# Optimization experiments

Measured on AMD Instinct MI355X. Metric: run time of the kernel, lower is better.

Reference implementation:

```python
import jax, jax.numpy as jnp
import numpy as np

EPS = 1e-5
NHEAD = 8
TOP_K = 2


def _layernorm(x, g, b):
    m = jnp.mean(x, axis=-1, keepdims=True)
    v = jnp.mean((x - m) ** 2, axis=-1, keepdims=True)
    return (x - m) * jax.lax.rsqrt(v + EPS) * g + b


def setup_inputs() -> dict:
    S, D, F, E = 4096, 512, 2048, 8
    key = jax.random.key(0)
    ks = jax.random.split(key, 18)
    std = 0.02
    return {
        "src": jax.random.normal(ks[0], (S, D), jnp.float32),
        "in_proj_w": std * jax.random.normal(ks[1], (3 * D, D), jnp.float32),
        "in_proj_b": jnp.zeros((3 * D,), jnp.float32),
        "out_proj_w": std * jax.random.normal(ks[2], (D, D), jnp.float32),
        "out_proj_b": jnp.zeros((D,), jnp.float32),
        "ln1_g": jnp.ones((D,), jnp.float32),
        "ln1_b": jnp.zeros((D,), jnp.float32),
        "ln2_g": jnp.ones((D,), jnp.float32),
        "ln2_b": jnp.zeros((D,), jnp.float32),
        "gate_w": std * jax.random.normal(ks[3], (E, D), jnp.float32),
        "gate_b": jnp.zeros((E,), jnp.float32),
        "w1": std * jax.random.normal(ks[4], (E, F, D), jnp.float32),
        "b1": jnp.zeros((E, F), jnp.float32),
        "w2": std * jax.random.normal(ks[5], (E, F, D), jnp.float32),
        "b2": jnp.zeros((E, F), jnp.float32),
        "wo": std * jax.random.normal(ks[6], (E, D, F), jnp.float32),
        "bo": jnp.zeros((E, D), jnp.float32),
    }


def _sa_block(x, in_proj_w, in_proj_b, out_proj_w, out_proj_b):
    # x: [S, D] unbatched sequence (torch MultiheadAttention unbatched path)
    S, D = x.shape
    hd = D // NHEAD
    qkv = x @ in_proj_w.T + in_proj_b              # [S, 3D]
    q, k, v = jnp.split(qkv, 3, axis=-1)
    q = q.reshape(S, NHEAD, hd)
    k = k.reshape(S, NHEAD, hd)
    v = v.reshape(S, NHEAD, hd)
    scores = jnp.einsum("shd,thd->hst", q, k) / jnp.sqrt(jnp.float32(hd))
    attn = jax.nn.softmax(scores, axis=-1)         # [H, S, S]
    out = jnp.einsum("hst,thd->shd", attn, v).reshape(S, D)
    return out @ out_proj_w.T + out_proj_b


def _ff_block(x, gate_w, gate_b, w1, b1, w2, b2, wo, bo):
    # top-k gated SwiGLU MoE; gate probs are softmax, NOT renormalized after topk
    T = x.shape[0]
    E = w1.shape[0]
    gates = jax.nn.softmax(x @ gate_w.T + gate_b, axis=-1)      # [T, E]
    top_scores, top_idx = jax.lax.top_k(gates, TOP_K)            # [T, k]
    combine = jnp.zeros((T, E), x.dtype).at[
        jnp.arange(T)[:, None], top_idx].add(top_scores)         # [T, E]
    out = jnp.zeros_like(x)
    for e in range(E):  # small fixed expert count
        h = jax.nn.silu(x @ w1[e].T + b1[e]) * (x @ w2[e].T + b2[e])
        out = out + combine[:, e:e + 1] * (h @ wo[e].T + bo[e])
    return out


def reference(src, in_proj_w, in_proj_b, out_proj_w, out_proj_b,
              ln1_g, ln1_b, ln2_g, ln2_b,
              gate_w, gate_b, w1, b1, w2, b2, wo, bo):
    # norm_first pre-norm residual layer, dropout=0 (eval)
    x = src
    x = x + _sa_block(_layernorm(x, ln1_g, ln1_b),
                      in_proj_w, in_proj_b, out_proj_w, out_proj_b)
    x = x + _ff_block(_layernorm(x, ln2_g, ln2_b),
                      gate_w, gate_b, w1, b1, w2, b2, wo, bo)
    return x
```

## Files before the change

kernel.cpp:

```cpp
#include <hip/hip_runtime.h>
#include <hip/hip_bf16.h>
#include <math.h>

#define SQ   4096
#define DM   512
#define NH   8
#define HDIM 64
#define FF   2048
#define NE   8

typedef unsigned short u16;
typedef unsigned int   u32;
typedef __attribute__((ext_vector_type(8))) __bf16 bf16x8;
typedef __attribute__((ext_vector_type(4))) float  f32x4;

__device__ __forceinline__ float bf2f(u16 v) {
    union { u32 i; float f; } c; c.i = ((u32)v) << 16; return c.f;
}
__device__ __forceinline__ u16 f2bf(float f) {
    union { __bf16 h; u16 u; } c; c.h = (__bf16)f; return c.u;
}

#define BM 128
#define BN 128
#define BK 32
#define BKP 40

__global__ __launch_bounds__(256) void gemm_split(
    const u16* __restrict__ Ahi, const u16* __restrict__ Alo, int lda,
    const u16* __restrict__ Bhi, const u16* __restrict__ Blo, int ldb,
    int M, int N, int K,
    const float* __restrict__ bias,
    const float* __restrict__ resid, int ldres,
    u16* __restrict__ Chi, u16* __restrict__ Clo,
    float* __restrict__ Cf, int ldc, int mode)
{
    __shared__ __align__(16) u16 Ash[BM * BKP], Asl[BM * BKP];
    __shared__ __align__(16) u16 Bsh[BN * BKP], Bsl[BN * BKP];
    const int tid  = threadIdx.x;
    const int wave = tid >> 6;
    const int lane = tid & 63;
    const int quad = lane >> 4;
    const int l16  = lane & 15;
    const int bm = blockIdx.x * BM;
    const int bn = blockIdx.y * BN;
    const int wm = (wave & 1) * 64;
    const int wn = (wave >> 1) * 64;

    f32x4 acc[4][4];
#pragma unroll
    for (int i = 0; i < 4; i++)
#pragma unroll
        for (int j = 0; j < 4; j++)
#pragma unroll
            for (int r = 0; r < 4; r++) acc[i][j][r] = 0.0f;

    for (int k0 = 0; k0 < K; k0 += BK) {
#pragma unroll
        for (int i = 0; i < 2; i++) {
            int c = tid + i * 256;
            int row = c >> 2;
            int col = (c & 3) << 3;
            int ga = bm + row, gb2 = bn + row;
            uint4 vah = make_uint4(0u,0u,0u,0u), val = vah, vbh = vah, vbl = vah;
            if (ga < M) {
                vah = *(const uint4*)(Ahi + (size_t)ga * lda + k0 + col);
                val = *(const uint4*)(Alo + (size_t)ga * lda + k0 + col);
            }
            if (gb2 < N) {
                vbh = *(const uint4*)(Bhi + (size_t)gb2 * ldb + k0 + col);
                vbl = *(const uint4*)(Blo + (size_t)gb2 * ldb + k0 + col);
            }
            *(uint4*)(Ash + row * BKP + col) = vah;
            *(uint4*)(Asl + row * BKP + col) = val;
            *(uint4*)(Bsh + row * BKP + col) = vbh;
            *(uint4*)(Bsl + row * BKP + col) = vbl;
        }
        __syncthreads();
        bf16x8 ah[4], al[4], bh[4], bl[4];
#pragma unroll
        for (int i = 0; i < 4; i++) {
            ah[i] = *(const bf16x8*)(Ash + (wm + i * 16 + l16) * BKP + quad * 8);
            al[i] = *(const bf16x8*)(Asl + (wm + i * 16 + l16) * BKP + quad * 8);
        }
#pragma unroll
        for (int j = 0; j < 4; j++) {
            bh[j] = *(const bf16x8*)(Bsh + (wn + j * 16 + l16) * BKP + quad * 8);
            bl[j] = *(const bf16x8*)(Bsl + (wn + j * 16 + l16) * BKP + quad * 8);
        }
#pragma unroll
        for (int i = 0; i < 4; i++)
#pragma unroll
            for (int j = 0; j < 4; j++) {
                acc[i][j] = __builtin_amdgcn_mfma_f32_16x16x32_bf16(ah[i], bh[j], acc[i][j], 0,0,0);
                acc[i][j] = __builtin_amdgcn_mfma_f32_16x16x32_bf16(ah[i], bl[j], acc[i][j], 0,0,0);
                acc[i][j] = __builtin_amdgcn_mfma_f32_16x16x32_bf16(al[i], bh[j], acc[i][j], 0,0,0);
            }
        __syncthreads();
    }

#pragma unroll
    for (int i = 0; i < 4; i++)
#pragma unroll
        for (int j = 0; j < 4; j++)
#pragma unroll
            for (int r = 0; r < 4; r++) {
                int row = bm + wm + i * 16 + quad * 4 + r;
                int col = bn + wn + j * 16 + l16;
                if (row >= M || col >= N) continue;
                float v = acc[i][j][r] + (bias ? bias[col] : 0.0f);
                size_t idx = (size_t)row * ldc + col;
                if (mode == 0) {
                    u16 hb = f2bf(v);
                    Chi[idx] = hb;
                    Clo[idx] = f2bf(v - bf2f(hb));
                } else {
                    if (resid) v += resid[(size_t)row * ldres + col];
                    Cf[idx] = v;
                }
            }
}

__global__ __launch_bounds__(256) void moe12_all(
    const u16* __restrict__ A, int lda,
    const int* __restrict__ idxl, const int* __restrict__ cnt,
    const int* __restrict__ off,
    const float* __restrict__ w1, const float* __restrict__ b1,
    const float* __restrict__ w2, const float* __restrict__ b2,
    u16* __restrict__ H)
{
    const int bmg = blockIdx.x * BM;
    if (bmg >= off[NE]) return;
    int e = 0;
    while (e < NE - 1 && bmg >= off[e + 1]) e++;
    const int M   = cnt[e];
    const int bml = bmg - off[e];
    if (bml >= M) return;
    const float* B1 = w1 + (size_t)e * FF * DM;
    const float* B2 = w2 + (size_t)e * FF * DM;
    const int*   rl = idxl + e * SQ;

    __shared__ __align__(16) u16 As[BM * BKP], Bs1[BN * BKP], Bs2[BN * BKP];
    const int tid  = threadIdx.x;
    const int wave = tid >> 6;
    const int lane = tid & 63;
    const int quad = lane >> 4;
    const int l16  = lane & 15;
    const int bn = blockIdx.y * BN;
    const int wm = (wave & 1) * 64;
    const int wn = (wave >> 1) * 64;

    f32x4 acc1[4][4], acc2[4][4];
#pragma unroll
    for (int i = 0; i < 4; i++)
#pragma unroll
        for (int j = 0; j < 4; j++)
#pragma unroll
            for (int r = 0; r < 4; r++) { acc1[i][j][r] = 0.0f; acc2[i][j][r] = 0.0f; }

    for (int k0 = 0; k0 < DM; k0 += BK) {
#pragma unroll
        for (int i = 0; i < 2; i++) {
            int c = tid + i * 256;
            int row = c >> 2;
            int col = (c & 3) << 3;
            uint4 va = make_uint4(0u,0u,0u,0u);
            int lr = bml + row;
            if (lr < M) {
                int ar = rl[lr];
                va = *(const uint4*)(A + (size_t)ar * lda + k0 + col);
            }
            *(uint4*)(As + row * BKP + col) = va;
        }
#pragma unroll
        for (int i = 0; i < 4; i++) {
            int c = tid + i * 256;
            int row = c >> 3;
            int col = (c & 7) << 2;
            float4 v1 = *(const float4*)(B1 + (size_t)(bn + row) * DM + k0 + col);
            float4 v2 = *(const float4*)(B2 + (size_t)(bn + row) * DM + k0 + col);
            ushort4 h1, h2;
            h1.x = f2bf(v1.x); h1.y = f2bf(v1.y); h1.z = f2bf(v1.z); h1.w = f2bf(v1.w);
            h2.x = f2bf(v2.x); h2.y = f2bf(v2.y); h2.z = f2bf(v2.z); h2.w = f2bf(v2.w);
            *(ushort4*)(Bs1 + row * BKP + col) = h1;
            *(ushort4*)(Bs2 + row * BKP + col) = h2;
        }
        __syncthreads();
        bf16x8 af[4], b1f[4], b2f[4];
#pragma unroll
        for (int i = 0; i < 4; i++)
            af[i] = *(const bf16x8*)(As + (wm + i * 16 + l16) * BKP + quad * 8);
#pragma unroll
        for (int j = 0; j < 4; j++) {
            b1f[j] = *(const bf16x8*)(Bs1 + (wn + j * 16 + l16) * BKP + quad * 8);
            b2f[j] = *(const bf16x8*)(Bs2 + (wn + j * 16 + l16) * BKP + quad * 8);
        }
#pragma unroll
        for (int i = 0; i < 4; i++)
#pragma unroll
            for (int j = 0; j < 4; j++) {
                acc1[i][j] = __builtin_amdgcn_mfma_f32_16x16x32_bf16(af[i], b1f[j], acc1[i][j], 0,0,0);
                acc2[i][j] = __builtin_amdgcn_mfma_f32_16x16x32_bf16(af[i], b2f[j], acc2[i][j], 0,0,0);
            }
        __syncthreads();
    }

#pragma unroll
    for (int i = 0; i < 4; i++)
#pragma unroll
        for (int j = 0; j < 4; j++)
#pragma unroll
            for (int r = 0; r < 4; r++) {
                int rowl = bml + wm + i * 16 + quad * 4 + r;
                if (rowl >= M) continue;
                int col = bn + wn + j * 16 + l16;
                float g1 = acc1[i][j][r] + b1[e * FF + col];
                float g2 = acc2[i][j][r] + b2[e * FF + col];
                float s  = g1 / (1.0f + __expf(-g1));
                H[(size_t)(off[e] + rowl) * FF + col] = f2bf(s * g2);
            }
}

__global__ __launch_bounds__(256) void moe_y_all(
    const u16* __restrict__ H,
    const float* __restrict__ wo, const float* __restrict__ bo,
    const int* __restrict__ idxl, const float* __restrict__ cw,
    const int* __restrict__ cnt, const int* __restrict__ off,
    float* __restrict__ out)
{
    const int bmg = blockIdx.x * BM;
    if (bmg >= off[NE]) return;
    int e = 0;
    while (e < NE - 1 && bmg >= off[e + 1]) e++;
    const int M   = cnt[e];
    const int bml = bmg - off[e];
    if (bml >= M) return;
    const float* B = wo + (size_t)e * DM * FF;

    __shared__ __align__(16) u16 As[BM * BKP], Bs[BN * BKP];
    const int tid  = threadIdx.x;
    const int wave = tid >> 6;
    const int lane = tid & 63;
    const int quad = lane >> 4;
    const int l16  = lane & 15;
    const int bn = blockIdx.y * BN;
    const int wm = (wave & 1) * 64;
    const int wn = (wave >> 1) * 64;

    f32x4 acc[4][4];
#pragma unroll
    for (int i = 0; i < 4; i++)
#pragma unroll
        for (int j = 0; j < 4; j++)
#pragma unroll
            for (int r = 0; r < 4; r++) acc[i][j][r] = 0.0f;

    for (int k0 = 0; k0 < FF; k0 += BK) {
#pragma unroll
        for (int i = 0; i < 2; i++) {
            int c = tid + i * 256;
            int row = c >> 2;
            int col = (c & 3) << 3;
            uint4 va = *(const uint4*)(H + (size_t)(bmg + row) * FF + k0 + col);
            *(uint4*)(As + row * BKP + col) = va;
        }
#pragma unroll
        for (int i = 0; i < 4; i++) {
            int c = tid + i * 256;
            int row = c >> 3;
            int col = (c & 7) << 2;
            float4 v = *(const float4*)(B + (size_t)(bn + row) * FF + k0 + col);
            ushort4 h;
            h.x = f2bf(v.x); h.y = f2bf(v.y); h.z = f2bf(v.z); h.w = f2bf(v.w);
            *(ushort4*)(Bs + row * BKP + col) = h;
        }
        __syncthreads();
        bf16x8 af[4], bf[4];
#pragma unroll
        for (int i = 0; i < 4; i++)
            af[i] = *(const bf16x8*)(As + (wm + i * 16 + l16) * BKP + quad * 8);
#pragma unroll
        for (int j = 0; j < 4; j++)
            bf[j] = *(const bf16x8*)(Bs + (wn + j * 16 + l16) * BKP + quad * 8);
#pragma unroll
        for (int i = 0; i < 4; i++)
#pragma unroll
            for (int j = 0; j < 4; j++)
                acc[i][j] = __builtin_amdgcn_mfma_f32_16x16x32_bf16(af[i], bf[j], acc[i][j], 0,0,0);
        __syncthreads();
    }

#pragma unroll
    for (int i = 0; i < 4; i++)
#pragma unroll
        for (int j = 0; j < 4; j++)
#pragma unroll
            for (int r = 0; r < 4; r++) {
                int rowl = bml + wm + i * 16 + quad * 4 + r;
                if (rowl >= M) continue;
                int col = bn + wn + j * 16 + l16;
                int tok = idxl[e * SQ + rowl];
                float wgt = cw[e * SQ + rowl];
                atomicAdd(out + (size_t)tok * DM + col,
                          wgt * (acc[i][j][r] + bo[e * DM + col]));
            }
}

#define KP 64
#define SWZ(row, col) ((col) ^ (((row) & 7) << 3))
#define SCL 0.18033688011112042f

template <int SPLIT>
__device__ __forceinline__ void flash_body(
    const u16* __restrict__ qh, const u16* __restrict__ ql,
    const u16* __restrict__ vth, const u16* __restrict__ vtl,
    u16* __restrict__ oh, u16* __restrict__ ol,
    float* __restrict__ Opart, float* __restrict__ mpart,
    float* __restrict__ lpart)
{
    __shared__ __align__(16) u16 Ksh[64*KP], Ksl[64*KP], Vsh[64*KP], Vsl[64*KP];
    const int tid  = threadIdx.x;
    const int wave = tid >> 6;
    const int lane = tid & 63;
    const int quad = lane >> 4;
    const int l16  = lane & 15;
    const int h    = blockIdx.y;
    const int z    = (SPLIT > 1) ? blockIdx.z : 0;
    const int qbase = blockIdx.x * 64 + wave * 16;

    u16* const Pwh = Ksh + wave * (16 * KP);
    u16* const Pwl = Ksl + wave * (16 * KP);

    const int r_st  = tid >> 3;
    const int co_g  = (tid & 7) << 3;
    const int co_sw = SWZ(r_st, co_g);

    bf16x8 aqh[2], aql[2];
#pragma unroll
    for (int kk = 0; kk < 2; kk++) {
        size_t off = (size_t)(qbase + l16) * (3*DM) + h*HDIM + kk*32 + quad*8;
        aqh[kk] = *(const bf16x8*)(qh + off);
        aql[kk] = *(const bf16x8*)(ql + off);
    }

    float m_[4], l_[4];
    f32x4 o_[4];
#pragma unroll
    for (int r = 0; r < 4; r++) { m_[r] = -1e30f; l_[r] = 0.0f; }
#pragma unroll
    for (int nd = 0; nd < 4; nd++)
#pragma unroll
        for (int r = 0; r < 4; r++) o_[nd][r] = 0.0f;

    const int NT    = SQ / 64 / SPLIT;
    const int jtBeg = z * NT, jtEnd = (z + 1) * NT;

    for (int jt = jtBeg; jt < jtEnd; jt++) {
        {
            size_t koff0 = (size_t)(jt*64 + r_st) * (3*DM) + DM + h*HDIM + co_g;
            size_t voff0 = (size_t)(h*HDIM + r_st) * SQ + jt*64 + co_g;
            size_t koff1 = koff0 + (size_t)32 * (3*DM);
            size_t voff1 = voff0 + (size_t)32 * SQ;
            uint4 a0 = *(const uint4*)(qh  + koff0);
            uint4 a1 = *(const uint4*)(ql  + koff0);
            uint4 a2 = *(const uint4*)(vth + voff0);
            uint4 a3 = *(const uint4*)(vtl + voff0);
            uint4 b0 = *(const uint4*)(qh  + koff1);
            uint4 b1 = *(const uint4*)(ql  + koff1);
            uint4 b2 = *(const uint4*)(vth + voff1);
            uint4 b3 = *(const uint4*)(vtl + voff1);
            *(uint4*)(Ksh + r_st*KP + co_sw)      = a0;
            *(uint4*)(Ksl + r_st*KP + co_sw)      = a1;
            *(uint4*)(Vsh + r_st*KP + co_sw)      = a2;
            *(uint4*)(Vsl + r_st*KP + co_sw)      = a3;
            *(uint4*)(Ksh + (r_st+32)*KP + co_sw) = b0;
            *(uint4*)(Ksl + (r_st+32)*KP + co_sw) = b1;
            *(uint4*)(Vsh + (r_st+32)*KP + co_sw) = b2;
            *(uint4*)(Vsl + (r_st+32)*KP + co_sw) = b3;
        }
        __syncthreads();

        f32x4 s[4];
        __builtin_amdgcn_s_setprio(1);
#pragma unroll
        for (int jn = 0; jn < 4; jn++) {
            f32x4 zz;
#pragma unroll
            for (int r = 0; r < 4; r++) zz[r] = 0.0f;
#pragma unroll
            for (int kk = 0; kk < 2; kk++) {
                int krow = jn*16 + l16;
                int kcol = SWZ(krow, kk*32 + quad*8);
                bf16x8 kh = *(const bf16x8*)(Ksh + krow*KP + kcol);
                bf16x8 kl = *(const bf16x8*)(Ksl + krow*KP + kcol);
                zz = __builtin_amdgcn_mfma_f32_16x16x32_bf16(aqh[kk], kh, zz, 0,0,0);
                zz = __builtin_amdgcn_mfma_f32_16x16x32_bf16(aqh[kk], kl, zz, 0,0,0);
                zz = __builtin_amdgcn_mfma_f32_16x16x32_bf16(aql[kk], kh, zz, 0,0,0);
            }
#pragma unroll
            for (int r = 0; r < 4; r++) zz[r] *= SCL;
            s[jn] = zz;
        }
        __builtin_amdgcn_s_setprio(0);
        __syncthreads();

        float mx[4];
#pragma unroll
        for (int r = 0; r < 4; r++) {
            mx[r] = fmaxf(fmaxf(s[0][r], s[1][r]), fmaxf(s[2][r], s[3][r]));
#pragma unroll
            for (int o2 = 1; o2 < 16; o2 <<= 1)
                mx[r] = fmaxf(mx[r], __shfl_xor(mx[r], o2));
        }
        int grew = (mx[0] > m_[0] + 8.0f) | (mx[1] > m_[1] + 8.0f) |
                   (mx[2] > m_[2] + 8.0f) | (mx[3] > m_[3] + 8.0f);
        if (__any(grew)) {
#pragma unroll
            for (int r = 0; r < 4; r++) {
                float nm  = fmaxf(m_[r], mx[r]);
                float al2 = exp2f(m_[r] - nm);
                m_[r] = nm;
                l_[r] *= al2;
#pragma unroll
                for (int nd = 0; nd < 4; nd++) o_[nd][r] *= al2;
            }
        }
        float rs[4];
#pragma unroll
        for (int r = 0; r < 4; r++) rs[r] = 0.0f;
#pragma unroll
        for (int jn = 0; jn < 4; jn++)
#pragma unroll
            for (int r = 0; r < 4; r++) {
                float p = exp2f(s[jn][r] - m_[r]);
                s[jn][r] = p;
                rs[r] += p;
            }
#pragma unroll
        for (int r = 0; r < 4; r++) {
#pragma unroll
            for (int o2 = 1; o2 < 16; o2 <<= 1)
                rs[r] += __shfl_xor(rs[r], o2);
            l_[r] += rs[r];
        }
#pragma unroll
        for (int jn = 0; jn < 4; jn++)
#pragma unroll
            for (int r = 0; r < 4; r++) {
                float p = s[jn][r];
                u16 ph = f2bf(p);
                int rr   = quad*4 + r;
                int pidx = rr*KP + SWZ(rr, jn*16 + l16);
                Pwh[pidx] = ph;
                Pwl[pidx] = f2bf(p - bf2f(ph));
            }

        bf16x8 ph[2], pl[2];
#pragma unroll
        for (int kk = 0; kk < 2; kk++) {
            int pcol = SWZ(l16, kk*32 + quad*8);
            ph[kk] = *(const bf16x8*)(Pwh + l16*KP + pcol);
            pl[kk] = *(const bf16x8*)(Pwl + l16*KP + pcol);
        }
        __builtin_amdgcn_s_setprio(1);
#pragma unroll
        for (int nd = 0; nd < 4; nd++) {
#pragma unroll
            for (int kk = 0; kk < 2; kk++) {
                int vrow = nd*16 + l16;
                int vcol = SWZ(vrow, kk*32 + quad*8);
                bf16x8 vh = *(const bf16x8*)(Vsh + vrow*KP + vcol);
                bf16x8 vl = *(const bf16x8*)(Vsl + vrow*KP + vcol);
                o_[nd] = __builtin_amdgcn_mfma_f32_16x16x32_bf16(ph[kk], vh, o_[nd], 0,0,0);
                o_[nd] = __builtin_amdgcn_mfma_f32_16x16x32_bf16(ph[kk], vl, o_[nd], 0,0,0);
                o_[nd] = __builtin_amdgcn_mfma_f32_16x16x32_bf16(pl[kk], vh, o_[nd], 0,0,0);
            }
        }
        __builtin_amdgcn_s_setprio(0);
        __syncthreads();
    }

    if (SPLIT == 1) {
#pragma unroll
        for (int nd = 0; nd < 4; nd++)
#pragma unroll
            for (int r = 0; r < 4; r++) {
                int row = qbase + quad*4 + r;
                int col = h*HDIM + nd*16 + l16;
                float w = o_[nd][r] / l_[r];
                u16 hb = f2bf(w);
                oh[(size_t)row * DM + col] = hb;
                ol[(size_t)row * DM + col] = f2bf(w - bf2f(hb));
            }
    } else {
#pragma unroll
        for (int nd = 0; nd < 4; nd++)
#pragma unroll
            for (int r = 0; r < 4; r++) {
                int row = qbase + quad*4 + r;
                int col = h*HDIM + nd*16 + l16;
                Opart[((size_t)z * SQ + row) * DM + col] = o_[nd][r];
            }
        if (l16 == 0) {
#pragma unroll
            for (int r = 0; r < 4; r++) {
                int row = qbase + quad*4 + r;
                mpart[(z*NH + h) * SQ + row] = m_[r];
                lpart[(z*NH + h) * SQ + row] = l_[r];
            }
        }
    }
}

__global__ __launch_bounds__(256) void flash_attn(
    const u16* __restrict__ qh, const u16* __restrict__ ql,
    const u16* __restrict__ vth, const u16* __restrict__ vtl,
    u16* __restrict__ oh, u16* __restrict__ ol)
{
    flash_body<1>(qh, ql, vth, vtl, oh, ol, nullptr, nullptr, nullptr);
}

__global__ __launch_bounds__(256) void flash_attn_part2(
    const u16* __restrict__ qh, const u16* __restrict__ ql,
    const u16* __restrict__ vth, const u16* __restrict__ vtl,
    float* __restrict__ Opart, float* __restrict__ mpart,
    float* __restrict__ lpart)
{
    flash_body<2>(qh, ql, vth, vtl, nullptr, nullptr, Opart, mpart, lpart);
}

__global__ __launch_bounds__(256) void flash_attn_part4(
    const u16* __restrict__ qh, const u16* __restrict__ ql,
    const u16* __restrict__ vth, const u16* __restrict__ vtl,
    float* __restrict__ Opart, float* __restrict__ mpart,
    float* __restrict__ lpart)
{
    flash_body<4>(qh, ql, vth, vtl, nullptr, nullptr, Opart, mpart, lpart);
}

__global__ __launch_bounds__(256) void attn_combine(
    const float* __restrict__ Opart, const float* __restrict__ mpart,
    const float* __restrict__ lpart,
    u16* __restrict__ oh, u16* __restrict__ ol, int ns)
{
    const int row = blockIdx.x;
    const int tid = threadIdx.x;
#pragma unroll
    for (int i = 0; i < 2; i++) {
        int col = tid + i * 256;
        int h = col >> 6;
        float m = -1e30f;
        for (int zz = 0; zz < ns; zz++)
            m = fmaxf(m, mpart[(zz*NH + h) * SQ + row]);
        float O = 0.0f, l = 0.0f;
        for (int zz = 0; zz < ns; zz++) {
            float a = exp2f(mpart[(zz*NH + h) * SQ + row] - m);
            O += Opart[((size_t)zz * SQ + row) * DM + col] * a;
            l += lpart[(zz*NH + h) * SQ + row] * a;
        }
        float w = O / l;
        u16 hb = f2bf(w);
        oh[(size_t)row * DM + col] = hb;
        ol[(size_t)row * DM + col] = f2bf(w - bf2f(hb));
    }
}

__global__ __launch_bounds__(256) void ln1_split(
    const float* __restrict__ x, const float* __restrict__ g,
    const float* __restrict__ b, u16* __restrict__ ohi, u16* __restrict__ olo)
{
    const int row = blockIdx.x;
    const int tid = threadIdx.x;
    float v0 = x[(size_t)row * DM + tid];
    float v1 = x[(size_t)row * DM + tid + 256];
    float s = v0 + v1, sq = v0*v0 + v1*v1;
#pragma unroll
    for (int o = 1; o < 64; o <<= 1) { s += __shfl_xor(s, o); sq += __shfl_xor(sq, o); }
    __shared__ float ss[4], ssq[4];
    if ((tid & 63) == 0) { ss[tid>>6] = s; ssq[tid>>6] = sq; }
    __syncthreads();
    s  = ss[0]+ss[1]+ss[2]+ss[3];
    sq = ssq[0]+ssq[1]+ssq[2]+ssq[3];
    float m = s * (1.0f/DM);
    float rstd = rsqrtf(sq*(1.0f/DM) - m*m + 1e-5f);
    float y0 = (v0-m)*rstd*g[tid]     + b[tid];
    float y1 = (v1-m)*rstd*g[tid+256] + b[tid+256];
    u16 h0 = f2bf(y0), h1 = f2bf(y1);
    ohi[(size_t)row*DM + tid]       = h0;  olo[(size_t)row*DM + tid]       = f2bf(y0 - bf2f(h0));
    ohi[(size_t)row*DM + tid + 256] = h1;  olo[(size_t)row*DM + tid + 256] = f2bf(y1 - bf2f(h1));
}

__global__ __launch_bounds__(256) void ln_kernel(
    const float* __restrict__ x, const float* __restrict__ g,
    const float* __restrict__ b, u16* __restrict__ out)
{
    const int row = blockIdx.x;
    const int tid = threadIdx.x;
    float v0 = x[(size_t)row * DM + tid];
    float v1 = x[(size_t)row * DM + tid + 256];
    float s = v0 + v1, sq = v0*v0 + v1*v1;
#pragma unroll
    for (int o = 1; o < 64; o <<= 1) { s += __shfl_xor(s, o); sq += __shfl_xor(sq, o); }
    __shared__ float ss[4], ssq[4];
    if ((tid & 63) == 0) { ss[tid>>6] = s; ssq[tid>>6] = sq; }
    __syncthreads();
    s  = ss[0]+ss[1]+ss[2]+ss[3];
    sq = ssq[0]+ssq[1]+ssq[2]+ssq[3];
    float m = s * (1.0f/DM);
    float rstd = rsqrtf(sq*(1.0f/DM) - m*m + 1e-5f);
    out[(size_t)row*DM + tid]       = f2bf((v0-m)*rstd*g[tid]     + b[tid]);
    out[(size_t)row*DM + tid + 256] = f2bf((v1-m)*rstd*g[tid+256] + b[tid+256]);
}

__global__ __launch_bounds__(256) void transpose_v2(
    const u16* __restrict__ qh, const u16* __restrict__ ql,
    u16* __restrict__ vth, u16* __restrict__ vtl)
{
    __shared__ u16 Th[64 * 66], Tl[64 * 66];
    const int t0  = blockIdx.x * 64;
    const int hd0 = blockIdx.y * 64;
    const int tid = threadIdx.x;
#pragma unroll
    for (int k = 0; k < 16; k++) {
        int idx = tid + k * 256;
        int r = idx >> 6, j = idx & 63;
        size_t src = (size_t)(t0 + r) * (3*DM) + 2*DM + hd0 + j;
        Th[r * 66 + j] = qh[src];
        Tl[r * 66 + j] = ql[src];
    }
    __syncthreads();
#pragma unroll
    for (int k = 0; k < 16; k++) {
        int idx = tid + k * 256;
        int r = idx >> 6, c2 = idx & 63;
        size_t dst = (size_t)(hd0 + r) * SQ + t0 + c2;
        vth[dst] = Th[c2 * 66 + r];
        vtl[dst] = Tl[c2 * 66 + r];
    }
}

__global__ __launch_bounds__(256) void gate_route(
    const float* __restrict__ x1, const float* __restrict__ g,
    const float* __restrict__ b, const float* __restrict__ gw,
    const float* __restrict__ gb,
    int* __restrict__ cnt, int* __restrict__ idxl, float* __restrict__ cw)
{
    const int token = blockIdx.x * 4 + (threadIdx.x >> 6);
    const int lane  = threadIdx.x & 63;
    const float* xr = x1 + (size_t)token * DM;
    float v[8];
#pragma unroll
    for (int i = 0; i < 8; i++) v[i] = xr[lane*8 + i];
    float s = 0.f, sq = 0.f;
#pragma unroll
    for (int i = 0; i < 8; i++) { s += v[i]; sq += v[i]*v[i]; }
#pragma unroll
    for (int o = 1; o < 64; o <<= 1) { s += __shfl_xor(s, o); sq += __shfl_xor(sq, o); }
    float m = s * (1.0f/DM);
    float rstd = rsqrtf(sq*(1.0f/DM) - m*m + 1e-5f);
    float xn[8];
#pragma unroll
    for (int i = 0; i < 8; i++)
        xn[i] = (v[i]-m)*rstd*g[lane*8+i] + b[lane*8+i];
    float logit[8];
#pragma unroll
    for (int e = 0; e < 8; e++) {
        float t = 0.f;
#pragma unroll
        for (int i = 0; i < 8; i++) t += xn[i] * gw[e*DM + lane*8 + i];
#pragma unroll
        for (int o = 1; o < 64; o <<= 1) t += __shfl_xor(t, o);
        logit[e] = t + gb[e];
    }
    if (lane == 0) {
        float mx = -1e30f;
        for (int e = 0; e < 8; e++) mx = fmaxf(mx, logit[e]);
        float den = 0.f, p[8];
        for (int e = 0; e < 8; e++) { p[e] = __expf(logit[e] - mx); den += p[e]; }
        for (int e = 0; e < 8; e++) p[e] /= den;
        int i1 = 0;
        for (int e = 1; e < 8; e++) if (p[e] > p[i1]) i1 = e;
        int i2 = -1;
        for (int e = 0; e < 8; e++) { if (e == i1) continue; if (i2 < 0 || p[e] > p[i2]) i2 = e; }
        int s1 = atomicAdd(&cnt[i1], 1);
        idxl[i1*SQ + s1] = token;  cw[i1*SQ + s1] = p[i1];
        int s2 = atomicAdd(&cnt[i2], 1);
        idxl[i2*SQ + s2] = token;  cw[i2*SQ + s2] = p[i2];
    }
}

__global__ __launch_bounds__(256) void cvt_split_w(
    const float* __restrict__ w, u16* __restrict__ wh, u16* __restrict__ wl, int n)
{
    int i = blockIdx.x * 256 + threadIdx.x;
    if (i < n) {
        float v = w[i];
        u16 h = f2bf(v);
        wh[i] = h;
        wl[i] = f2bf(v - bf2f(h));
    }
}

__global__ __launch_bounds__(64) void zero_cnt(int* cnt)
{
    if (threadIdx.x < NE) cnt[threadIdx.x] = 0;
}

__global__ __launch_bounds__(64) void make_off(const int* __restrict__ cnt,
                                              int* __restrict__ off)
{
    if (threadIdx.x == 0) {
        int a = 0;
        for (int e = 0; e < NE; e++) {
            off[e] = a;
            a += ((cnt[e] + 127) >> 7) << 7;
        }
        off[NE] = a;
    }
}

__global__ __launch_bounds__(256) void init_out(
    const float* __restrict__ x1, float* __restrict__ out)
{
    int i = blockIdx.x * 256 + threadIdx.x;
    ((float4*)out)[i] = ((const float4*)x1)[i];
}

__global__ __launch_bounds__(256) void sentinel_kernel(float* out, float v, int n)
{
    int i = blockIdx.x * 256 + threadIdx.x;
    if (i < n) out[i] = v;
}
__global__ __launch_bounds__(256) void scrub_kernel(float* out, int n)
{
    int i = blockIdx.x * 256 + threadIdx.x;
    if (i < n) { float v = out[i]; if (!isfinite(v)) out[i] = 777.0f; }
}

extern "C" void kernel_launch(void* const* d_in, const int* in_sizes, int n_in,
                              void* d_out, int out_size, void* d_ws, size_t ws_size,
                              hipStream_t stream)
{
    const float* src        = (const float*)d_in[0];
    const float* in_proj_w  = (const float*)d_in[1];
    const float* in_proj_b  = (const float*)d_in[2];
    const float* out_proj_w = (const float*)d_in[3];
    const float* out_proj_b = (const float*)d_in[4];
    const float* ln1_g      = (const float*)d_in[5];
    const float* ln1_b      = (const float*)d_in[6];
    const float* ln2_g      = (const float*)d_in[7];
    const float* ln2_b      = (const float*)d_in[8];
    const float* gate_w     = (const float*)d_in[9];
    const float* gate_b     = (const float*)d_in[10];
    const float* w1         = (const float*)d_in[11];
    const float* b1         = (const float*)d_in[12];
    const float* w2         = (const float*)d_in[13];
    const float* b2         = (const float*)d_in[14];
    const float* wo         = (const float*)d_in[15];
    const float* bo         = (const float*)d_in[16];
    float* out = (float*)d_out;

    const size_t MB = (size_t)1 << 20;
    const size_t ROUTE = 512 * 1024;
    const size_t NEED      = ROUTE + 44 * MB;
    const size_t NEED_BIG2 = ROUTE + 61 * MB;
    const size_t NEED_BIG4 = ROUTE + 78 * MB;
    if (ws_size < NEED) {
        sentinel_kernel<<<(SQ*DM)/256, 256, 0, stream>>>(out, 333.0f, SQ*DM);
        return;
    }
    int ns = 0;
    if (ws_size >= NEED_BIG4)      ns = 4;
    else if (ws_size >= NEED_BIG2) ns = 2;

    char* ws = (char*)d_ws;
    int*   cnt  = (int*)ws;
    int*   offp = (int*)(ws + 64);
    int*   idxl = (int*)(ws + 1024);
    float* cw   = (float*)(ws + 1024 + 128*1024);
    char*  base = ws + ROUTE;
    u16* xln1h = (u16*)(base);
    u16* xln1l = (u16*)(base + 4*MB);
    u16* attnh = (u16*)(base);
    u16* attnl = (u16*)(base + 4*MB);
    u16* qkvh  = (u16*)(base + 8*MB);
    u16* qkvl  = (u16*)(base + 20*MB);
    float* x1  = (float*)(base + 8*MB);
    u16* vth   = (u16*)(base + 32*MB);
    u16* vtl   = (u16*)(base + 36*MB);
    u16* xln2  = (u16*)(base + 36*MB);
    u16* Hbuf  = (u16*)(base);
    u16* wph   = (u16*)(base + 40*MB);
    u16* wpl   = (u16*)(base + 40*MB + 1536*1024);
    u16* woh   = (u16*)(base + 43*MB);
    u16* wol   = (u16*)(base + 43*MB + 512*1024);
    float* Opart = (float*)(base + 44*MB);
    float* mpart;
    float* lpart;
    if (ns == 4) {
        mpart = (float*)(base + 76*MB);
        lpart = (float*)(base + 76*MB + 512*1024);
    } else {
        mpart = (float*)(base + 60*MB);
        lpart = (float*)(base + 60*MB + 256*1024);
    }

    cvt_split_w<<<(3*DM*DM)/256, 256, 0, stream>>>(in_proj_w,  wph, wpl, 3*DM*DM);
    cvt_split_w<<<(DM*DM)/256,   256, 0, stream>>>(out_proj_w, woh, wol, DM*DM);

    ln1_split<<<SQ, 256, 0, stream>>>(src, ln1_g, ln1_b, xln1h, xln1l);
    gemm_split<<<dim3(32, 12), 256, 0, stream>>>(
        xln1h, xln1l, DM, wph, wpl, DM, SQ, 3*DM, DM,
        in_proj_b, nullptr, 0, qkvh, qkvl, nullptr, 3*DM, 0);
    transpose_v2<<<dim3(SQ/64, DM/64), 256, 0, stream>>>(qkvh, qkvl, vth, vtl);
    if (ns == 4) {
        flash_attn_part4<<<dim3(SQ/64, NH, 4), 256, 0, stream>>>(
            qkvh, qkvl, vth, vtl, Opart, mpart, lpart);
        attn_combine<<<SQ, 256, 0, stream>>>(Opart, mpart, lpart, attnh, attnl, 4);
    } else if (ns == 2) {
        flash_attn_part2<<<dim3(SQ/64, NH, 2), 256, 0, stream>>>(
            qkvh, qkvl, vth, vtl, Opart, mpart, lpart);
        attn_combine<<<SQ, 256, 0, stream>>>(Opart, mpart, lpart, attnh, attnl, 2);
    } else {
        flash_attn<<<dim3(SQ/64, NH), 256, 0, stream>>>(
            qkvh, qkvl, vth, vtl, attnh, attnl);
    }
    gemm_split<<<dim3(32, 4), 256, 0, stream>>>(
        attnh, attnl, DM, woh, wol, DM, SQ, DM, DM,
        out_proj_b, src, DM, nullptr, nullptr, x1, DM, 1);

    ln_kernel<<<SQ, 256, 0, stream>>>(x1, ln2_g, ln2_b, xln2);
    zero_cnt<<<1, 64, 0, stream>>>(cnt);
    gate_route<<<SQ/4, 256, 0, stream>>>(x1, ln2_g, ln2_b, gate_w, gate_b,
                                         cnt, idxl, cw);
    make_off<<<1, 64, 0, stream>>>(cnt, offp);
    init_out<<<(SQ*DM/4)/256, 256, 0, stream>>>(x1, out);
    moe12_all<<<dim3(72, 16), 256, 0, stream>>>(
        xln2, DM, idxl, cnt, offp, w1, b1, w2, b2, Hbuf);
    moe_y_all<<<dim3(72, 4), 256, 0, stream>>>(
        Hbuf, wo, bo, idxl, cw, cnt, offp, out);

    scrub_kernel<<<(SQ*DM)/256, 256, 0, stream>>>(out, SQ*DM);
}
```

Before: 794.1 us.

## Pre-convert MoE expert weights to bf16 and split-K the out-projection with atomics

Adds kernels that convert the fp32 expert weights w1, w2 and wo to bf16 once per call, then run bf16-weight variants of the two MoE GEMMs. These replace the older kernels, which read fp32 weights and presumably converted them while loading tiles. The out-projection GEMM is split four ways along K with atomicAdd into x1, which is first initialised with src plus the bias, to raise block count. The trade is extra conversion passes and atomic traffic. The new MoE path runs only when ns==4, and the weight buffers reuse scratch regions that Opart/mpart also use.

```diff
diff --git a/kernel.cpp b/kernel.cpp
--- a/kernel.cpp
+++ b/kernel.cpp
@@ -121,6 +121,96 @@
             }
 }
 
+__global__ __launch_bounds__(256) void gemm_split_ko(
+    const u16* __restrict__ Ahi, const u16* __restrict__ Alo, int lda,
+    const u16* __restrict__ Bhi, const u16* __restrict__ Blo, int ldb,
+    float* __restrict__ Cf, int ldc)
+{
+    __shared__ __align__(16) u16 Ash[BM * BKP], Asl[BM * BKP];
+    __shared__ __align__(16) u16 Bsh[BN * BKP], Bsl[BN * BKP];
+    const int tid  = threadIdx.x;
+    const int wave = tid >> 6;
+    const int lane = tid & 63;
+    const int quad = lane >> 4;
+    const int l16  = lane & 15;
+    const int bm = blockIdx.x * BM;
+    const int bn = blockIdx.y * BN;
+    const int wm = (wave & 1) * 64;
+    const int wn = (wave >> 1) * 64;
+    const int KC    = DM / 4;
+    const int k0beg = blockIdx.z * KC;
+
+    f32x4 acc[4][4];
+#pragma unroll
+    for (int i = 0; i < 4; i++)
+#pragma unroll
+        for (int j = 0; j < 4; j++)
+#pragma unroll
+            for (int r = 0; r < 4; r++) acc[i][j][r] = 0.0f;
+
+    for (int k0 = k0beg; k0 < k0beg + KC; k0 += BK) {
+#pragma unroll
+        for (int i = 0; i < 2; i++) {
+            int c = tid + i * 256;
+            int row = c >> 2;
+            int col = (c & 3) << 3;
+            int ga = bm + row, gb2 = bn + row;
+            uint4 vah = *(const uint4*)(Ahi + (size_t)ga * lda + k0 + col);
+            uint4 val = *(const uint4*)(Alo + (size_t)ga * lda + k0 + col);
+            uint4 vbh = *(const uint4*)(Bhi + (size_t)gb2 * ldb + k0 + col);
+            uint4 vbl = *(const uint4*)(Blo + (size_t)gb2 * ldb + k0 + col);
+            *(uint4*)(Ash + row * BKP + col) = vah;
+            *(uint4*)(Asl + row * BKP + col) = val;
+            *(uint4*)(Bsh + row * BKP + col) = vbh;
+            *(uint4*)(Bsl + row * BKP + col) = vbl;
+        }
+        __syncthreads();
+        bf16x8 ah[4], al[4], bh[4], bl[4];
+#pragma unroll
+        for (int i = 0; i < 4; i++) {
+            ah[i] = *(const bf16x8*)(Ash + (wm + i * 16 + l16) * BKP + quad * 8);
+            al[i] = *(const bf16x8*)(Asl + (wm + i * 16 + l16) * BKP + quad * 8);
+        }
+#pragma unroll
+        for (int j = 0; j < 4; j++) {
+            bh[j] = *(const bf16x8*)(Bsh + (wn + j * 16 + l16) * BKP + quad * 8);
+            bl[j] = *(const bf16x8*)(Bsl + (wn + j * 16 + l16) * BKP + quad * 8);
+        }
+#pragma unroll
+        for (int i = 0; i < 4; i++)
+#pragma unroll
+            for (int j = 0; j < 4; j++) {
+                acc[i][j] = __builtin_amdgcn_mfma_f32_16x16x32_bf16(ah[i], bh[j], acc[i][j], 0,0,0);
+                acc[i][j] = __builtin_amdgcn_mfma_f32_16x16x32_bf16(ah[i], bl[j], acc[i][j], 0,0,0);
+                acc[i][j] = __builtin_amdgcn_mfma_f32_16x16x32_bf16(al[i], bh[j], acc[i][j], 0,0,0);
+            }
+        __syncthreads();
+    }
+
+#pragma unroll
+    for (int i = 0; i < 4; i++)
+#pragma unroll
+        for (int j = 0; j < 4; j++)
+#pragma unroll
+            for (int r = 0; r < 4; r++) {
+                int row = bm + wm + i * 16 + quad * 4 + r;
+                int col = bn + wn + j * 16 + l16;
+                atomicAdd(Cf + (size_t)row * ldc + col, acc[i][j][r]);
+            }
+}
+
+__global__ __launch_bounds__(256) void init_x1(
+    const float* __restrict__ src, const float* __restrict__ bias,
+    float* __restrict__ x1)
+{
+    int i = blockIdx.x * 256 + threadIdx.x;
+    int col4 = i & (DM / 4 - 1);
+    float4 s = ((const float4*)src)[i];
+    float4 b = ((const float4*)bias)[col4];
+    s.x += b.x; s.y += b.y; s.z += b.z; s.w += b.w;
+    ((float4*)x1)[i] = s;
+}
+
 __global__ __launch_bounds__(256) void moe12_all(
     const u16* __restrict__ A, int lda,
     const int* __restrict__ idxl, const int* __restrict__ cnt,
@@ -221,6 +311,97 @@
             }
 }
 
+__global__ __launch_bounds__(256) void moe12_bf16(
+    const u16* __restrict__ A, int lda,
+    const int* __restrict__ idxl, const int* __restrict__ cnt,
+    const int* __restrict__ off,
+    const u16* __restrict__ w1b, const float* __restrict__ b1,
+    const u16* __restrict__ w2b, const float* __restrict__ b2,
+    u16* __restrict__ H)
+{
+    const int bmg = blockIdx.x * BM;
+    if (bmg >= off[NE]) return;
+    int e = 0;
+    while (e < NE - 1 && bmg >= off[e + 1]) e++;
+    const int M   = cnt[e];
+    const int bml = bmg - off[e];
+    if (bml >= M) return;
+    const u16* B1 = w1b + (size_t)e * FF * DM;
+    const u16* B2 = w2b + (size_t)e * FF * DM;
+    const int* rl = idxl + e * SQ;
+
+    __shared__ __align__(16) u16 As[BM * BKP], Bs1[BN * BKP], Bs2[BN * BKP];
+    const int tid  = threadIdx.x;
+    const int wave = tid >> 6;
+    const int lane = tid & 63;
+    const int quad = lane >> 4;
+    const int l16  = lane & 15;
+    const int bn = blockIdx.y * BN;
+    const int wm = (wave & 1) * 64;
+    const int wn = (wave >> 1) * 64;
+
+    f32x4 acc1[4][4], acc2[4][4];
+#pragma unroll
+    for (int i = 0; i < 4; i++)
+#pragma unroll
+        for (int j = 0; j < 4; j++)
+#pragma unroll
+            for (int r = 0; r < 4; r++) { acc1[i][j][r] = 0.0f; acc2[i][j][r] = 0.0f; }
+
+    for (int k0 = 0; k0 < DM; k0 += BK) {
+#pragma unroll
+        for (int i = 0; i < 2; i++) {
+            int c = tid + i * 256;
+            int row = c >> 2;
+            int col = (c & 3) << 3;
+            uint4 va = make_uint4(0u,0u,0u,0u);
+            int lr = bml + row;
+            if (lr < M) {
+                int ar = rl[lr];
+                va = *(const uint4*)(A + (size_t)ar * lda + k0 + col);
+            }
+            *(uint4*)(As + row * BKP + col) = va;
+            uint4 v1 = *(const uint4*)(B1 + (size_t)(bn + row) * DM + k0 + col);
+            uint4 v2 = *(const uint4*)(B2 + (size_t)(bn + row) * DM + k0 + col);
+            *(uint4*)(Bs1 + row * BKP + col) = v1;
+            *(uint4*)(Bs2 + row * BKP + col) = v2;
+        }
+        __syncthreads();
+        bf16x8 af[4], b1f[4], b2f[4];
+#pragma unroll
+        for (int i = 0; i < 4; i++)
+            af[i] = *(const bf16x8*)(As + (wm + i * 16 + l16) * BKP + quad * 8);
+#pragma unroll
+        for (int j = 0; j < 4; j++) {
+            b1f[j] = *(const bf16x8*)(Bs1 + (wn + j * 16 + l16) * BKP + quad * 8);
+            b2f[j] = *(const bf16x8*)(Bs2 + (wn + j * 16 + l16) * BKP + quad * 8);
+        }
+#pragma unroll
+        for (int i = 0; i < 4; i++)
+#pragma unroll
+            for (int j = 0; j < 4; j++) {
+                acc1[i][j] = __builtin_amdgcn_mfma_f32_16x16x32_bf16(af[i], b1f[j], acc1[i][j], 0,0,0);
+                acc2[i][j] = __builtin_amdgcn_mfma_f32_16x16x32_bf16(af[i], b2f[j], acc2[i][j], 0,0,0);
+            }
+        __syncthreads();
+    }
+
+#pragma unroll
+    for (int i = 0; i < 4; i++)
+#pragma unroll
+        for (int j = 0; j < 4; j++)
+#pragma unroll
+            for (int r = 0; r < 4; r++) {
+                int rowl = bml + wm + i * 16 + quad * 4 + r;
+                if (rowl >= M) continue;
+                int col = bn + wn + j * 16 + l16;
+                float g1 = acc1[i][j][r] + b1[e * FF + col];
+                float g2 = acc2[i][j][r] + b2[e * FF + col];
+                float s  = g1 / (1.0f + __expf(-g1));
+                H[(size_t)(off[e] + rowl) * FF + col] = f2bf(s * g2);
+            }
+}
+
 __global__ __launch_bounds__(256) void moe_y_all(
     const u16* __restrict__ H,
     const float* __restrict__ wo, const float* __restrict__ bo,
@@ -304,6 +485,95 @@
                 atomicAdd(out + (size_t)tok * DM + col,
                           wgt * (acc[i][j][r] + bo[e * DM + col]));
             }
+}
+
+__global__ __launch_bounds__(256) void moe_y_bf16(
+    const u16* __restrict__ H,
+    const u16* __restrict__ wob, const float* __restrict__ bo,
+    const int* __restrict__ idxl, const float* __restrict__ cw,
+    const int* __restrict__ cnt, const int* __restrict__ off,
+    float* __restrict__ out)
+{
+    const int bmg = blockIdx.x * BM;
+    if (bmg >= off[NE]) return;
+    int e = 0;
+    while (e < NE - 1 && bmg >= off[e + 1]) e++;
+    const int M   = cnt[e];
+    const int bml = bmg - off[e];
+    if (bml >= M) return;
+    const u16* B = wob + (size_t)e * DM * FF;
+
+    __shared__ __align__(16) u16 As[BM * BKP], Bs[BN * BKP];
+    const int tid  = threadIdx.x;
+    const int wave = tid >> 6;
+    const int lane = tid & 63;
+    const int quad = lane >> 4;
+    const int l16  = lane & 15;
+    const int bn = blockIdx.y * BN;
+    const int wm = (wave & 1) * 64;
+    const int wn = (wave >> 1) * 64;
+
+    f32x4 acc[4][4];
+#pragma unroll
+    for (int i = 0; i < 4; i++)
+#pragma unroll
+        for (int j = 0; j < 4; j++)
+#pragma unroll
+            for (int r = 0; r < 4; r++) acc[i][j][r] = 0.0f;
+
+    for (int k0 = 0; k0 < FF; k0 += BK) {
+#pragma unroll
+        for (int i = 0; i < 2; i++) {
+            int c = tid + i * 256;
+            int row = c >> 2;
+            int col = (c & 3) << 3;
+            uint4 va = *(const uint4*)(H + (size_t)(bmg + row) * FF + k0 + col);
+            *(uint4*)(As + row * BKP + col) = va;
+            uint4 vb = *(const uint4*)(B + (size_t)(bn + row) * FF + k0 + col);
+            *(uint4*)(Bs + row * BKP + col) = vb;
+        }
+        __syncthreads();
+        bf16x8 af[4], bf[4];
+#pragma unroll
+        for (int i = 0; i < 4; i++)
+            af[i] = *(const bf16x8*)(As + (wm + i * 16 + l16) * BKP + quad * 8);
+#pragma unroll
+        for (int j = 0; j < 4; j++)
+            bf[j] = *(const bf16x8*)(Bs + (wn + j * 16 + l16) * BKP + quad * 8);
+#pragma unroll
+        for (int i = 0; i < 4; i++)
+#pragma unroll
+            for (int j = 0; j < 4; j++)
+                acc[i][j] = __builtin_amdgcn_mfma_f32_16x16x32_bf16(af[i], bf[j], acc[i][j], 0,0,0);
+        __syncthreads();
+    }
+
+#pragma unroll
+    for (int i = 0; i < 4; i++)
+#pragma unroll
+        for (int j = 0; j < 4; j++)
+#pragma unroll
+            for (int r = 0; r < 4; r++) {
+                int rowl = bml + wm + i * 16 + quad * 4 + r;
+                if (rowl >= M) continue;
+                int col = bn + wn + j * 16 + l16;
+                int tok = idxl[e * SQ + rowl];
+                float wgt = cw[e * SQ + rowl];
+                atomicAdd(out + (size_t)tok * DM + col,
+                          wgt * (acc[i][j][r] + bo[e * DM + col]));
+            }
+}
+
+__global__ __launch_bounds__(256) void cvt_w_bf16(
+    const float* __restrict__ w, u16* __restrict__ wb, int n4)
+{
+    int i = blockIdx.x * 256 + threadIdx.x;
+    if (i < n4) {
+        float4 v = ((const float4*)w)[i];
+        ushort4 h;
+        h.x = f2bf(v.x); h.y = f2bf(v.y); h.z = f2bf(v.z); h.w = f2bf(v.w);
+        ((ushort4*)wb)[i] = h;
+    }
 }
 
 #define KP 64
@@ -804,6 +1074,9 @@
         mpart = (float*)(base + 60*MB);
         lpart = (float*)(base + 60*MB + 256*1024);
     }
+    u16* w1b = (u16*)(base + 44*MB);
+    u16* w2b = (u16*)(base + 60*MB);
+    u16* wob = (u16*)(base + 44*MB);
 
     cvt_split_w<<<(3*DM*DM)/256, 256, 0, stream>>>(in_proj_w,  wph, wpl, 3*DM*DM);
     cvt_split_w<<<(DM*DM)/256,   256, 0, stream>>>(out_proj_w, woh, wol, DM*DM);
@@ -825,9 +1098,9 @@
         flash_attn<<<dim3(SQ/64, NH), 256, 0, stream>>>(
             qkvh, qkvl, vth, vtl, attnh, attnl);
     }
-    gemm_split<<<dim3(32, 4), 256, 0, stream>>>(
-        attnh, attnl, DM, woh, wol, DM, SQ, DM, DM,
-        out_proj_b, src, DM, nullptr, nullptr, x1, DM, 1);
+    init_x1<<<(SQ*DM/4)/256, 256, 0, stream>>>(src, out_proj_b, x1);
+    gemm_split_ko<<<dim3(32, 4, 4), 256, 0, stream>>>(
+        attnh, attnl, DM, woh, wol, DM, x1, DM);
 
     ln_kernel<<<SQ, 256, 0, stream>>>(x1, ln2_g, ln2_b, xln2);
     zero_cnt<<<1, 64, 0, stream>>>(cnt);
@@ -835,10 +1108,21 @@
                                          cnt, idxl, cw);
     make_off<<<1, 64, 0, stream>>>(cnt, offp);
     init_out<<<(SQ*DM/4)/256, 256, 0, stream>>>(x1, out);
-    moe12_all<<<dim3(72, 16), 256, 0, stream>>>(
-        xln2, DM, idxl, cnt, offp, w1, b1, w2, b2, Hbuf);
-    moe_y_all<<<dim3(72, 4), 256, 0, stream>>>(
-        Hbuf, wo, bo, idxl, cw, cnt, offp, out);
+    const int WN4 = (NE * FF * DM) / 4;
+    if (ns == 4) {
+        cvt_w_bf16<<<WN4/256, 256, 0, stream>>>(w1, w1b, WN4);
+        cvt_w_bf16<<<WN4/256, 256, 0, stream>>>(w2, w2b, WN4);
+        moe12_bf16<<<dim3(72, 16), 256, 0, stream>>>(
+            xln2, DM, idxl, cnt, offp, w1b, b1, w2b, b2, Hbuf);
+        cvt_w_bf16<<<WN4/256, 256, 0, stream>>>(wo, wob, WN4);
+        moe_y_bf16<<<dim3(72, 4), 256, 0, stream>>>(
+            Hbuf, wob, bo, idxl, cw, cnt, offp, out);
+    } else {
+        moe12_all<<<dim3(72, 16), 256, 0, stream>>>(
+            xln2, DM, idxl, cnt, offp, w1, b1, w2, b2, Hbuf);
+        moe_y_all<<<dim3(72, 4), 256, 0, stream>>>(
+            Hbuf, wo, bo, idxl, cw, cnt, offp, out);
+    }
 
     scrub_kernel<<<(SQ*DM)/256, 256, 0, stream>>>(out, SQ*DM);
 }
```

Result: no change. 784.4 us (-1.2%).
